# Performance work log

Hardware: AMD Instinct MI355X
Metric: run time of the kernel (lower is better)

The kernel has to match this reference:

```python
import jax, jax.numpy as jnp
import numpy as np

B, N, D, H, NDIMS, NS = 4, 1024, 512, 8, 3, 1
HD = D // H


def setup_inputs() -> dict:
    key = jax.random.key(0)
    ks = jax.random.split(key, 10)
    x = jax.random.normal(ks[0], (B, N, D), dtype=jnp.float32)
    coords = jax.random.normal(ks[1], (B, N, NDIMS), dtype=jnp.float32)
    # pad last 64 key positions in half the batch
    key_padding_mask = jnp.zeros((B, N), dtype=bool).at[: B // 2, -64:].set(True)
    s = 1.0 / np.sqrt(D)
    Wqkv = jax.random.normal(ks[2], (3 * D, D), dtype=jnp.float32) * s  # torch Linear weight [out,in]
    Wout = jax.random.normal(ks[3], (D, D), dtype=jnp.float32) * s
    bout = jnp.zeros((D,), dtype=jnp.float32)
    fin = NDIMS + 1  # num_dims>1 -> dist channel appended
    W1 = jax.random.normal(ks[4], (H * 4, fin), dtype=jnp.float32) / np.sqrt(fin)
    b1 = jnp.zeros((H * 4,), dtype=jnp.float32)
    W2 = jax.random.normal(ks[5], (H, H * 4), dtype=jnp.float32) / np.sqrt(H * 4)
    b2 = jnp.zeros((H,), dtype=jnp.float32)
    bias_alpha = jax.random.normal(ks[6], (1,), dtype=jnp.float32)
    return dict(x=x, coords=coords, key_padding_mask=key_padding_mask,
                bias_alpha=bias_alpha, W1=W1, b1=b1, W2=W2, b2=b2,
                Wqkv=Wqkv, Wout=Wout, bout=bout)


def reference(x, coords, key_padding_mask, bias_alpha, W1, b1, W2, b2, Wqkv, Wout, bout):
    scale = HD ** (-0.5)
    qkv = x @ Wqkv.T  # [B,N,3D]
    q, k, v = jnp.split(qkv, 3, axis=-1)
    q = q.reshape(B, N, H, HD).transpose(0, 2, 1, 3)  # [B,H,N,HD]
    k = k.reshape(B, N, H, HD).transpose(0, 2, 1, 3)
    v = v.reshape(B, N, H, HD).transpose(0, 2, 1, 3)

    dpos = coords[:, :, None, :] - coords[:, None, :, :]  # [B,N,N,ndims]
    dist = jnp.linalg.norm(dpos, axis=-1, keepdims=True)
    dpos = jnp.concatenate([dpos, dist], axis=-1)  # [B,N,N,ndims+1]
    h = jax.nn.gelu(dpos @ W1.T + b1, approximate=False)
    bias = (h @ W2.T + b2).transpose(0, 3, 1, 2)  # [B,H,N,N]
    # zero bias rows/cols for special tokens
    valid = jnp.arange(N) >= NS
    bias = bias * (valid[:, None] & valid[None, :])[None, None]

    dots = jnp.einsum('bhid,bhjd->bhij', q, k) * scale
    logits = dots + bias_alpha[0] * bias
    logits = jnp.where(key_padding_mask[:, None, None, :], -jnp.inf, logits)
    attn = jax.nn.softmax(logits, axis=-1)
    out = jnp.einsum('bhij,bhjd->bhid', attn, v)
    out = out.transpose(0, 2, 1, 3).reshape(B, N, D)
    return out @ Wout.T + bout, attn
```

## Files before the change

### kernel.cpp

```cpp
#include <hip/hip_runtime.h>
#include <hip/hip_fp16.h>
#include <stdint.h>
#include <math.h>

#define B_  4
#define N_  1024
#define D_  512
#define H_  8
#define HD_ 64

typedef short s16x8 __attribute__((ext_vector_type(8)));
typedef float f32x4 __attribute__((ext_vector_type(4)));
typedef float f32x2 __attribute__((ext_vector_type(2)));
typedef __fp16 f16x2 __attribute__((ext_vector_type(2)));

__device__ __forceinline__ unsigned short f2bf(float f) {
    unsigned u = __float_as_uint(f);
    u += 0x7fffu + ((u >> 16) & 1u);
    return (unsigned short)(u >> 16);
}
__device__ __forceinline__ float bf2f(unsigned short h) {
    return __uint_as_float(((unsigned)h) << 16);
}

__device__ __forceinline__ float fast_gelu(float x) {
    float ax = fabsf(x) * 0.7071067811865476f;
    float t  = __builtin_amdgcn_rcpf(fmaf(0.3275911f, ax, 1.0f));
    float e  = __expf(-ax * ax);
    float poly = t * fmaf(t, fmaf(t, fmaf(t, fmaf(t, 1.061405429f, -1.453152027f),
                                          1.421413741f), -0.284496736f), 0.254829592f);
    float erfv = 1.0f - poly * e;
    float s = copysignf(erfv, x);
    return 0.5f * x * (1.0f + s);
}

__global__ void k_split(const float* __restrict__ s, unsigned short* __restrict__ h,
                        unsigned short* __restrict__ l, int n) {
    int i = blockIdx.x * 256 + threadIdx.x;
    if (i < n) {
        float x = s[i];
        unsigned short hb = f2bf(x);
        h[i] = hb;
        l[i] = f2bf(x - bf2f(hb));
    }
}

__global__ void k_mask_detect(const unsigned char* __restrict__ m, int* __restrict__ flag) {
    __shared__ int s;
    if (threadIdx.x == 0) s = 0;
    __syncthreads();
    int found = 0;
    for (int i = threadIdx.x; i < B_ * N_; i += 256)
        if ((i & 3) && m[i]) found = 1;
    if (found) atomicOr(&s, 1);
    __syncthreads();
    if (threadIdx.x == 0) flag[0] = s;
}

__global__ __launch_bounds__(256) void k_gemm3(
    const unsigned short* __restrict__ Ah, const unsigned short* __restrict__ Al,
    const unsigned short* __restrict__ Bwh, const unsigned short* __restrict__ Bwl,
    float* __restrict__ C, const float* __restrict__ bias, int M, int Nn, int K)
{
    constexpr int BM = 64, BN = 128, BK = 64;
    __shared__ unsigned short At[BM * BK];
    __shared__ unsigned short Bt[BN * BK];
    const int tid = threadIdx.x, lane = tid & 63, wid = tid >> 6;
    const int m0 = blockIdx.x * BM, n0 = blockIdx.y * BN;
    const int wm = wid >> 1, wn = wid & 1;
    f32x4 acc[2][4] = {};
    const unsigned short* Aps[3] = {Ah, Ah, Al};
    const unsigned short* Bps[3] = {Bwh, Bwl, Bwh};

    for (int combo = 0; combo < 3; ++combo) {
        const unsigned short* __restrict__ Ap = Aps[combo];
        const unsigned short* __restrict__ Bp = Bps[combo];
        for (int k0 = 0; k0 < K; k0 += BK) {
            s16x8 sa[2], sb[4];
            #pragma unroll
            for (int r = 0; r < 2; ++r) {
                int s = r * 256 + tid, row = s >> 3, c8 = s & 7;
                sa[r] = *(const s16x8*)(Ap + (size_t)(m0 + row) * K + k0 + c8 * 8);
            }
            #pragma unroll
            for (int r = 0; r < 4; ++r) {
                int s = r * 256 + tid, row = s >> 3, c8 = s & 7;
                sb[r] = *(const s16x8*)(Bp + (size_t)(n0 + row) * K + k0 + c8 * 8);
            }
            __syncthreads();
            #pragma unroll
            for (int r = 0; r < 2; ++r) { int s = r * 256 + tid; *(s16x8*)(At + s * 8) = sa[r]; }
            #pragma unroll
            for (int r = 0; r < 4; ++r) { int s = r * 256 + tid; *(s16x8*)(Bt + s * 8) = sb[r]; }
            __syncthreads();
            #pragma unroll
            for (int kk = 0; kk < BK; kk += 32) {
                s16x8 a[2], bb[4];
                #pragma unroll
                for (int fm = 0; fm < 2; ++fm)
                    a[fm] = *(const s16x8*)(At + (wm * 32 + fm * 16 + (lane & 15)) * BK + kk + (lane >> 4) * 8);
                #pragma unroll
                for (int fn = 0; fn < 4; ++fn)
                    bb[fn] = *(const s16x8*)(Bt + (wn * 64 + fn * 16 + (lane & 15)) * BK + kk + (lane >> 4) * 8);
                #pragma unroll
                for (int fm = 0; fm < 2; ++fm)
                    #pragma unroll
                    for (int fn = 0; fn < 4; ++fn)
                        acc[fm][fn] = __builtin_amdgcn_mfma_f32_16x16x32_bf16(a[fm], bb[fn], acc[fm][fn], 0, 0, 0);
            }
        }
    }
    #pragma unroll
    for (int fm = 0; fm < 2; ++fm)
        #pragma unroll
        for (int fn = 0; fn < 4; ++fn)
            #pragma unroll
            for (int r = 0; r < 4; ++r) {
                int row  = m0 + wm * 32 + fm * 16 + (lane >> 4) * 4 + r;
                int coln = n0 + wn * 64 + fn * 16 + (lane & 15);
                float v = acc[fm][fn][r];
                if (bias) v += bias[coln];
                C[(size_t)row * Nn + coln] = v;
            }
}

__global__ void k_rearrange(const float* __restrict__ qkv, unsigned short* __restrict__ qp,
                            unsigned short* __restrict__ kp) {
    int t = blockIdx.x * 256 + threadIdx.x;
    int d = t & 63, n = (t >> 6) & 1023, h = (t >> 16) & 7, b = t >> 19;
    const float* src = qkv + ((size_t)(b * N_ + n)) * (3 * D_) + h * HD_ + d;
    float q = src[0], k = src[D_];
    unsigned short qh = f2bf(q), ql = f2bf(q - bf2f(qh));
    unsigned short kh = f2bf(k), kl = f2bf(k - bf2f(kh));
    size_t base = ((size_t)(b * H_ + h) * N_ + n) * 128;
    qp[base + d] = qh; qp[base + 64 + d] = ql;
    kp[base + d] = kh; kp[base + 64 + d] = kl;
}

__global__ void k_vtrans(const float* __restrict__ qkv, unsigned short* __restrict__ vT) {
    __shared__ unsigned short T[64][65];
    int n0 = blockIdx.x * 64, h = blockIdx.y, b = blockIdx.z;
    int tid = threadIdx.x;
    #pragma unroll
    for (int rep = 0; rep < 16; ++rep) {
        int idx = rep * 256 + tid;
        int nl = idx >> 6, d = idx & 63;
        T[nl][d] = f2bf(qkv[((size_t)(b * N_ + n0 + nl)) * (3 * D_) + 2 * D_ + h * HD_ + d]);
    }
    __syncthreads();
    #pragma unroll
    for (int rep = 0; rep < 16; ++rep) {
        int idx = rep * 256 + tid;
        int dl = idx >> 6, nl = idx & 63;
        vT[((size_t)(b * H_ + h) * HD_ + dl) * N_ + n0 + nl] = T[nl][dl];
    }
}

__global__ void k_nodeproj(const float* __restrict__ coords, const float* __restrict__ W1,
                           unsigned short* __restrict__ Pt) {
    int t = blockIdx.x * 256 + threadIdx.x;
    int bn = t & 4095, c = t >> 12;
    const float* cc = coords + (size_t)bn * 3;
    float v = 32.f * (W1[c * 4] * cc[0] + W1[c * 4 + 1] * cc[1] + W1[c * 4 + 2] * cc[2]);
    __half hv = __float2half(v);
    Pt[t] = *(unsigned short*)&hv;
}

__global__ __launch_bounds__(256) void k_bias(
    const float* __restrict__ coords, const float* __restrict__ alpha,
    const float* __restrict__ W1, const float* __restrict__ b1,
    const float* __restrict__ W2, const float* __restrict__ b2,
    const unsigned short* __restrict__ Pt,
    unsigned short* __restrict__ biasH)
{
    __shared__ unsigned short sPj[32 * 256];
    __shared__ float lut[512];
    __shared__ float SPi[32], swd32[32], sb2f[8];
    __shared__ unsigned short sW2h[8 * 32];
    const int tid = threadIdx.x;
    const int bid = blockIdx.x;
    const int j0 = (bid & 3) * 256;
    const int i  = (bid >> 2) & 1023;
    const int b  = bid >> 12;

    {
        float xk = (tid - 128) * 0.03125f;
        float g0 = fast_gelu(xk);
        float g1 = fast_gelu(xk + 0.03125f);
        lut[tid * 2]     = g0;
        lut[tid * 2 + 1] = g1 - g0;
    }
    if (tid < 32) {
        const float* ci = coords + ((size_t)b * N_ + i) * 3;
        float w0 = W1[tid * 4], w1 = W1[tid * 4 + 1], w2 = W1[tid * 4 + 2], w3 = W1[tid * 4 + 3];
        SPi[tid]   = 32.f * (w0 * ci[0] + w1 * ci[1] + w2 * ci[2] + b1[tid]) + 128.f;
        swd32[tid] = 32.f * w3;
    }
    if (tid < 8) sb2f[tid] = b2[tid];
    {
        __half hv = __float2half(W2[tid]);
        sW2h[tid] = *(unsigned short*)&hv;
    }
    {
        #pragma unroll
        for (int p = 0; p < 4; ++p) {
            int idx = p * 256 + tid;
            int row = idx >> 5, off = (idx & 31) * 8;
            *(s16x8*)(sPj + row * 256 + off) =
                *(const s16x8*)(Pt + (size_t)row * (B_ * N_) + b * N_ + j0 + off);
        }
    }
    __syncthreads();

    const int j = j0 + tid;
    const float* ci = coords + ((size_t)b * N_ + i) * 3;
    const float* cj = coords + ((size_t)b * N_ + j) * 3;
    float dx = ci[0] - cj[0], dy = ci[1] - cj[1], dz = ci[2] - cj[2];
    float dist = sqrtf(dx * dx + dy * dy + dz * dz);

    float acc[8];
    #pragma unroll
    for (int h = 0; h < 8; ++h) acc[h] = 0.f;

    #pragma unroll 1
    for (int g = 0; g < 4; ++g) {
        f16x2 gh[4];
        float gprev = 0.f;
        #pragma unroll
        for (int cc = 0; cc < 8; ++cc) {
            int c = g * 8 + cc;
            unsigned short u = sPj[c * 256 + tid];
            float pj = __half2float(*(const __half*)&u);
            float t  = fmaf(swd32[c], dist, SPi[c] - pj);
            float tc = fminf(fmaxf(t, 0.f), 255.f);
            float fi = floorf(tc);
            int   ii = (int)fi;
            float fr = tc - fi;
            f32x2 vs = *(const f32x2*)(lut + ii * 2);
            float gg = fmaf(fr, vs[1], vs[0]);
            float xb = fmaf(t, 0.03125f, -4.f);
            gg = (t > 254.f) ? xb : gg;
            if (cc & 1) gh[cc >> 1] = __builtin_amdgcn_cvt_pkrtz(gprev, gg);
            else        gprev = gg;
        }
        #pragma unroll
        for (int h = 0; h < 8; ++h) {
            const f16x2* wp = (const f16x2*)(sW2h + h * 32 + g * 8);
            acc[h] = __builtin_amdgcn_fdot2(gh[0], wp[0], acc[h], false);
            acc[h] = __builtin_amdgcn_fdot2(gh[1], wp[1], acc[h], false);
            acc[h] = __builtin_amdgcn_fdot2(gh[2], wp[2], acc[h], false);
            acc[h] = __builtin_amdgcn_fdot2(gh[3], wp[3], acc[h], false);
        }
    }

    float vfac = (i >= 1 && j >= 1) ? alpha[0] : 0.f;
    #pragma unroll
    for (int h = 0; h < 8; ++h) {
        __half hv = __float2half(vfac * (acc[h] + sb2f[h]));
        biasH[(((size_t)(b * H_ + h)) * N_ + i) * N_ + j] = *(unsigned short*)&hv;
    }
}

__global__ __launch_bounds__(256, 3) void k_attn(
    const unsigned short* __restrict__ qp, const unsigned short* __restrict__ kp,
    const unsigned short* __restrict__ vT,
    const unsigned short* __restrict__ biasH,
    float* __restrict__ attnout,
    const unsigned char* __restrict__ mraw, const int* __restrict__ flag,
    unsigned short* __restrict__ avh, unsigned short* __restrict__ avl)
{
    __shared__ s16x8 pool16[2048];
    __shared__ unsigned char smask[N_];
    __shared__ float redm[16][4];
    __shared__ float reds[16][4];
    const int tid = threadIdx.x, lane = tid & 63, wid = tid >> 6;

    int flat = blockIdx.x + 64 * (blockIdx.y + 8 * blockIdx.z);
    int swz  = (flat & 7) * 256 + (flat >> 3);
    const int i0 = (swz & 63) * 16;
    const int h  = (swz >> 6) & 7;
    const int b  = swz >> 9;
    const size_t bh = (size_t)(b * H_ + h);
    const int g = lane >> 4;
    const int cl = lane & 15;

    if (flag[0] != 0) {
        for (int i2 = tid; i2 < N_; i2 += 256) smask[i2] = mraw[b * N_ + i2];
    } else {
        const int* mi = (const int*)mraw;
        for (int i2 = tid; i2 < N_; i2 += 256) smask[i2] = (unsigned char)(mi[b * N_ + i2] != 0);
    }

    const unsigned short* qrow = qp + (bh * N_ + i0 + cl) * 128 + g * 8;
    s16x8 aqh0 = *(const s16x8*)(qrow);
    s16x8 aqh1 = *(const s16x8*)(qrow + 32);
    s16x8 aql0 = *(const s16x8*)(qrow + 64);
    s16x8 aql1 = *(const s16x8*)(qrow + 96);

    int soff[4];
    #pragma unroll
    for (int p = 0; p < 4; ++p) {
        int o = p * 4096 + tid * 16;
        int row = o >> 8, offl = o & 255;
        soff[p] = row * 128 + ((offl ^ ((row & 7) << 4)) >> 1);
    }
    const unsigned short* kbase = kp + bh * (size_t)N_ * 128;

    const int lr = wid * 16 + cl;
    int rdoff[4];
    #pragma unroll
    for (int f = 0; f < 4; ++f)
        rdoff[f] = lr * 256 + ((g * 16 + f * 64) ^ ((lr & 7) << 4));

    char* poolb = (char*)pool16;

    {
        s16x8 st[4];
        #pragma unroll
        for (int p = 0; p < 4; ++p) st[p] = *(const s16x8*)(kbase + soff[p]);
        #pragma unroll
        for (int p = 0; p < 4; ++p) *(s16x8*)(poolb + p * 4096 + tid * 16) = st[p];
    }
    __syncthreads();

    f32x4 acc[16];
    #pragma unroll
    for (int c = 0; c < 16; ++c) {
        s16x8 st[4];
        if (c < 15) {
            const unsigned short* cb = kbase + (size_t)(c + 1) * 8192;
            #pragma unroll
            for (int p = 0; p < 4; ++p) st[p] = *(const s16x8*)(cb + soff[p]);
        }
        char* kb = poolb + (c & 1) * 16384;
        s16x8 k0 = *(const s16x8*)(kb + rdoff[0]);
        s16x8 k1 = *(const s16x8*)(kb + rdoff[1]);
        s16x8 k2 = *(const s16x8*)(kb + rdoff[2]);
        s16x8 k3 = *(const s16x8*)(kb + rdoff[3]);
        f32x4 a = {0.f, 0.f, 0.f, 0.f};
        a = __builtin_amdgcn_mfma_f32_16x16x32_bf16(aqh0, k0, a, 0, 0, 0);
        a = __builtin_amdgcn_mfma_f32_16x16x32_bf16(aqh1, k1, a, 0, 0, 0);
        a = __builtin_amdgcn_mfma_f32_16x16x32_bf16(aqh0, k2, a, 0, 0, 0);
        a = __builtin_amdgcn_mfma_f32_16x16x32_bf16(aqh1, k3, a, 0, 0, 0);
        a = __builtin_amdgcn_mfma_f32_16x16x32_bf16(aql0, k0, a, 0, 0, 0);
        a = __builtin_amdgcn_mfma_f32_16x16x32_bf16(aql1, k1, a, 0, 0, 0);
        acc[c] = a;
        if (c < 15) {
            char* wb = poolb + ((c + 1) & 1) * 16384;
            #pragma unroll
            for (int p = 0; p < 4; ++p) *(s16x8*)(wb + p * 4096 + tid * 16) = st[p];
        }
        __syncthreads();
    }

    {
        unsigned short* bl = (unsigned short*)poolb;
        const unsigned short* bsrc = biasH + (bh * N_ + i0) * N_;
        #pragma unroll
        for (int p2 = 0; p2 < 8; ++p2) {
            int idx = p2 * 256 + tid;
            *(s16x8*)(bl + idx * 8) = *(const s16x8*)(bsrc + (size_t)idx * 8);
        }
    }
    __syncthreads();

    const float scale = 0.125f;
    const unsigned short* bl = (const unsigned short*)poolb;
    #pragma unroll
    for (int j = 0; j < 16; ++j) {
        const int col = (j * 4 + wid) * 16 + cl;
        const bool mj = (smask[col] != 0);
        #pragma unroll
        for (int r = 0; r < 4; ++r) {
            unsigned short u = bl[(g * 4 + r) * 1024 + col];
            float bv = __half2float(*(const __half*)&u);
            acc[j][r] = mj ? -1e30f : fmaf(acc[j][r], scale, bv);
        }
    }

    float m[4];
    #pragma unroll
    for (int r = 0; r < 4; ++r) {
        float mm = acc[0][r];
        #pragma unroll
        for (int j = 1; j < 16; ++j) mm = fmaxf(mm, acc[j][r]);
        m[r] = mm;
    }
    #pragma unroll
    for (int msk = 1; msk < 16; msk <<= 1)
        #pragma unroll
        for (int r = 0; r < 4; ++r) m[r] = fmaxf(m[r], __shfl_xor(m[r], msk));
    if (cl == 0)
        #pragma unroll
        for (int r = 0; r < 4; ++r) redm[g * 4 + r][wid] = m[r];
    __syncthreads();
    #pragma unroll
    for (int r = 0; r < 4; ++r) {
        int row = g * 4 + r;
        m[r] = fmaxf(fmaxf(redm[row][0], redm[row][1]), fmaxf(redm[row][2], redm[row][3]));
    }

    float s[4] = {0.f, 0.f, 0.f, 0.f};
    #pragma unroll
    for (int j = 0; j < 16; ++j)
        #pragma unroll
        for (int r = 0; r < 4; ++r) {
            float e = __expf(acc[j][r] - m[r]);
            acc[j][r] = e;
            s[r] += e;
        }
    #pragma unroll
    for (int msk = 1; msk < 16; msk <<= 1)
        #pragma unroll
        for (int r = 0; r < 4; ++r) s[r] += __shfl_xor(s[r], msk);
    if (cl == 0)
        #pragma unroll
        for (int r = 0; r < 4; ++r) reds[g * 4 + r][wid] = s[r];
    __syncthreads();
    float sinv[4];
    #pragma unroll
    for (int r = 0; r < 4; ++r) {
        int row = g * 4 + r;
        sinv[r] = 1.0f / (reds[row][0] + reds[row][1] + reds[row][2] + reds[row][3]);
    }

    float* gattn = attnout + (bh * N_ + i0) * N_;
    char* Pb = poolb;
    #pragma unroll
    for (int j = 0; j < 16; ++j) {
        const int col = (j * 4 + wid) * 16 + cl;
        #pragma unroll
        for (int r = 0; r < 4; ++r) {
            const int row = g * 4 + r;
            float e = acc[j][r];
            gattn[(size_t)row * N_ + col] = e * sinv[r];
            int byte = row * 2048 + ((col * 2) ^ ((row & 7) << 4));
            *(unsigned short*)(Pb + byte) = f2bf(e);
        }
    }
    __syncthreads();

    {
        const int d0 = wid * 16;
        f32x4 acc2 = {0.f, 0.f, 0.f, 0.f};
        const unsigned short* vrow = vT + (bh * HD_ + d0 + cl) * N_ + g * 8;
        const int rowA = cl;
        const int swzb = (rowA & 7) << 4;
        for (int kk = 0; kk < N_; kk += 32) {
            s16x8 bfrag = *(const s16x8*)(vrow + kk);
            int byte = rowA * 2048 + (((kk + g * 8) * 2) ^ swzb);
            s16x8 af = *(const s16x8*)(Pb + byte);
            acc2 = __builtin_amdgcn_mfma_f32_16x16x32_bf16(af, bfrag, acc2, 0, 0, 0);
        }
        #pragma unroll
        for (int r = 0; r < 4; ++r) {
            const int row = g * 4 + r;
            const int dd = d0 + cl;
            float v = acc2[r] * sinv[r];
            unsigned short hv = f2bf(v);
            size_t o = ((size_t)(b * N_) + i0 + row) * D_ + h * HD_ + dd;
            avh[o] = hv;
            avl[o] = f2bf(v - bf2f(hv));
        }
    }
}

extern "C" void kernel_launch(void* const* d_in, const int* in_sizes, int n_in,
                              void* d_out, int out_size, void* d_ws, size_t ws_size,
                              hipStream_t stream) {
    (void)in_sizes; (void)n_in; (void)out_size; (void)ws_size;
    const float* x      = (const float*)d_in[0];
    const float* coords = (const float*)d_in[1];
    const unsigned char* kpm = (const unsigned char*)d_in[2];
    const float* alpha  = (const float*)d_in[3];
    const float* W1     = (const float*)d_in[4];
    const float* b1     = (const float*)d_in[5];
    const float* W2     = (const float*)d_in[6];
    const float* b2     = (const float*)d_in[7];
    const float* Wqkv   = (const float*)d_in[8];
    const float* Wout   = (const float*)d_in[9];
    const float* bout   = (const float*)d_in[10];

    float* out  = (float*)d_out;
    float* attn = out + (size_t)B_ * N_ * D_;

    char* w = (char*)d_ws;
    auto alloc = [&](size_t bytes) { char* p = w; w += (bytes + 255) & ~(size_t)255; return p; };
    const size_t SZ_X  = (size_t)B_ * N_ * D_;
    const size_t SZ_WQ = (size_t)3 * D_ * D_;
    const size_t SZ_WO = (size_t)D_ * D_;

    unsigned short* wo_hi = (unsigned short*)alloc(SZ_WO * 2);
    unsigned short* wo_lo = (unsigned short*)alloc(SZ_WO * 2);
    unsigned short* qp = (unsigned short*)alloc((size_t)B_ * H_ * N_ * 128 * 2);
    unsigned short* kp = (unsigned short*)alloc((size_t)B_ * H_ * N_ * 128 * 2);
    unsigned short* vT = (unsigned short*)alloc((size_t)B_ * H_ * HD_ * N_ * 2);
    unsigned short* av_hi = (unsigned short*)alloc(SZ_X * 2);
    unsigned short* av_lo = (unsigned short*)alloc(SZ_X * 2);
    unsigned short* Pt = (unsigned short*)alloc((size_t)32 * B_ * N_ * 2);
    int* flag = (int*)alloc(256);

    char* uni = (char*)alloc(0);
    unsigned short* x_hi = (unsigned short*)uni;
    unsigned short* x_lo = x_hi + SZ_X;
    unsigned short* wq_hi = x_lo + SZ_X;
    unsigned short* wq_lo = wq_hi + SZ_WQ;
    float* qkv = (float*)(wq_lo + SZ_WQ);
    unsigned short* biasH = (unsigned short*)uni;

    k_split<<<(int)((SZ_X + 255) / 256), 256, 0, stream>>>(x, x_hi, x_lo, (int)SZ_X);
    k_split<<<(int)((SZ_WQ + 255) / 256), 256, 0, stream>>>(Wqkv, wq_hi, wq_lo, (int)SZ_WQ);
    k_split<<<(int)((SZ_WO + 255) / 256), 256, 0, stream>>>(Wout, wo_hi, wo_lo, (int)SZ_WO);
    k_mask_detect<<<1, 256, 0, stream>>>(kpm, flag);
    k_nodeproj<<<(32 * B_ * N_) / 256, 256, 0, stream>>>(coords, W1, Pt);
    k_gemm3<<<dim3(64, 12), 256, 0, stream>>>(x_hi, x_lo, wq_hi, wq_lo, qkv, nullptr,
                                              B_ * N_, 3 * D_, D_);
    k_rearrange<<<(B_ * H_ * N_ * HD_) / 256, 256, 0, stream>>>(qkv, qp, kp);
    k_vtrans<<<dim3(16, H_, B_), 256, 0, stream>>>(qkv, vT);
    k_bias<<<(B_ * N_ * N_) / 256, 256, 0, stream>>>(coords, alpha, W1, b1, W2, b2, Pt, biasH);
    k_attn<<<dim3(64, H_, B_), 256, 0, stream>>>(qp, kp, vT, biasH, attn, kpm, flag, av_hi, av_lo);
    k_gemm3<<<dim3(64, 4), 256, 0, stream>>>(av_hi, av_lo, wo_hi, wo_lo, out, bout,
                                             B_ * N_, D_, D_);
}
```

Before: 242.5 us.

## Load GEMM and attention tiles directly into LDS; nontemporal attn stores

Replaces register-staged global-to-LDS copies with `__builtin_amdgcn_global_load_lds` direct transfers in the split-bf16 GEMM, the K-tile double buffer and the bias tile load of the attention kernel. In the attention loop, the next K chunk is now issued straight into the alternate buffer before the current chunk's MFMAs. The large fp32 attention-probability output is written with nontemporal stores to reduce cache pollution. The attention kernel's occupancy hint goes from 3 to 4 blocks per CU, which tightens the register budget. Correctness depends on the compiler inserting the needed vmcnt waits before the barriers.

```diff
diff --git a/kernel.cpp b/kernel.cpp
--- a/kernel.cpp
+++ b/kernel.cpp
@@ -13,6 +13,12 @@
 typedef float f32x4 __attribute__((ext_vector_type(4)));
 typedef float f32x2 __attribute__((ext_vector_type(2)));
 typedef __fp16 f16x2 __attribute__((ext_vector_type(2)));
+
+typedef const __attribute__((address_space(1))) void* gas1p;
+typedef __attribute__((address_space(3))) void* las3p;
+__device__ __forceinline__ void gload16(const void* g, void* l) {
+    __builtin_amdgcn_global_load_lds((gas1p)g, (las3p)l, 16, 0, 0);
+}
 
 __device__ __forceinline__ unsigned short f2bf(float f) {
     unsigned u = __float_as_uint(f);
@@ -76,22 +82,17 @@
         const unsigned short* __restrict__ Ap = Aps[combo];
         const unsigned short* __restrict__ Bp = Bps[combo];
         for (int k0 = 0; k0 < K; k0 += BK) {
-            s16x8 sa[2], sb[4];
+            __syncthreads();
             #pragma unroll
             for (int r = 0; r < 2; ++r) {
                 int s = r * 256 + tid, row = s >> 3, c8 = s & 7;
-                sa[r] = *(const s16x8*)(Ap + (size_t)(m0 + row) * K + k0 + c8 * 8);
+                gload16(Ap + (size_t)(m0 + row) * K + k0 + c8 * 8, At + s * 8);
             }
             #pragma unroll
             for (int r = 0; r < 4; ++r) {
                 int s = r * 256 + tid, row = s >> 3, c8 = s & 7;
-                sb[r] = *(const s16x8*)(Bp + (size_t)(n0 + row) * K + k0 + c8 * 8);
+                gload16(Bp + (size_t)(n0 + row) * K + k0 + c8 * 8, Bt + s * 8);
             }
-            __syncthreads();
-            #pragma unroll
-            for (int r = 0; r < 2; ++r) { int s = r * 256 + tid; *(s16x8*)(At + s * 8) = sa[r]; }
-            #pragma unroll
-            for (int r = 0; r < 4; ++r) { int s = r * 256 + tid; *(s16x8*)(Bt + s * 8) = sb[r]; }
             __syncthreads();
             #pragma unroll
             for (int kk = 0; kk < BK; kk += 32) {
@@ -261,7 +262,7 @@
     }
 }
 
-__global__ __launch_bounds__(256, 3) void k_attn(
+__global__ __launch_bounds__(256, 4) void k_attn(
     const unsigned short* __restrict__ qp, const unsigned short* __restrict__ kp,
     const unsigned short* __restrict__ vT,
     const unsigned short* __restrict__ biasH,
@@ -314,23 +315,20 @@
 
     char* poolb = (char*)pool16;
 
-    {
-        s16x8 st[4];
-        #pragma unroll
-        for (int p = 0; p < 4; ++p) st[p] = *(const s16x8*)(kbase + soff[p]);
-        #pragma unroll
-        for (int p = 0; p < 4; ++p) *(s16x8*)(poolb + p * 4096 + tid * 16) = st[p];
-    }
+    #pragma unroll
+    for (int p = 0; p < 4; ++p)
+        gload16(kbase + soff[p], poolb + p * 4096 + tid * 16);
     __syncthreads();
 
     f32x4 acc[16];
     #pragma unroll
     for (int c = 0; c < 16; ++c) {
-        s16x8 st[4];
         if (c < 15) {
             const unsigned short* cb = kbase + (size_t)(c + 1) * 8192;
+            char* wb = poolb + ((c + 1) & 1) * 16384;
             #pragma unroll
-            for (int p = 0; p < 4; ++p) st[p] = *(const s16x8*)(cb + soff[p]);
+            for (int p = 0; p < 4; ++p)
+                gload16(cb + soff[p], wb + p * 4096 + tid * 16);
         }
         char* kb = poolb + (c & 1) * 16384;
         s16x8 k0 = *(const s16x8*)(kb + rdoff[0]);
@@ -345,21 +343,16 @@
         a = __builtin_amdgcn_mfma_f32_16x16x32_bf16(aql0, k0, a, 0, 0, 0);
         a = __builtin_amdgcn_mfma_f32_16x16x32_bf16(aql1, k1, a, 0, 0, 0);
         acc[c] = a;
-        if (c < 15) {
-            char* wb = poolb + ((c + 1) & 1) * 16384;
-            #pragma unroll
-            for (int p = 0; p < 4; ++p) *(s16x8*)(wb + p * 4096 + tid * 16) = st[p];
-        }
         __syncthreads();
     }
 
     {
+        const unsigned short* bsrc = biasH + (bh * N_ + i0) * N_;
         unsigned short* bl = (unsigned short*)poolb;
-        const unsigned short* bsrc = biasH + (bh * N_ + i0) * N_;
         #pragma unroll
         for (int p2 = 0; p2 < 8; ++p2) {
             int idx = p2 * 256 + tid;
-            *(s16x8*)(bl + idx * 8) = *(const s16x8*)(bsrc + (size_t)idx * 8);
+            gload16(bsrc + (size_t)idx * 8, bl + idx * 8);
         }
     }
     __syncthreads();
@@ -433,7 +426,7 @@
         for (int r = 0; r < 4; ++r) {
             const int row = g * 4 + r;
             float e = acc[j][r];
-            gattn[(size_t)row * N_ + col] = e * sinv[r];
+            __builtin_nontemporal_store(e * sinv[r], &gattn[(size_t)row * N_ + col]);
             int byte = row * 2048 + ((col * 2) ^ ((row & 7) << 4));
             *(unsigned short*)(Pb + byte) = f2bf(e);
         }
```

Measured after the change: 237.6 us, median of 2. -2.0%, faster.
